# Kernel tuning notes

Hardware: AMD Instinct MI355X
Metric: run time of the kernel (lower is better)

Reference implementation:

```python
import jax, jax.numpy as jnp
import numpy as np

N, E, F_IN, HID, H, G = 50000, 800000, 128, 128, 4, 64
D = HID // H  # per-head dim = 32


def setup_inputs() -> dict:
    key = jax.random.key(0)
    ks = jax.random.split(key, 24)
    s = 0.05
    x = jax.random.normal(ks[0], (N, F_IN), dtype=jnp.float32)
    edge_index = jax.random.randint(ks[1], (2, E), 0, N, dtype=jnp.int64)
    batch = jnp.sort(jax.random.randint(ks[2], (N,), 0, G, dtype=jnp.int64))
    p = {}
    # layer 1: in F_IN -> H*D, layer 2: in HID -> H*D; each conv has q,k,v,skip linears (bias=True)
    names = ['Wq1', 'Wk1', 'Wv1', 'Ws1', 'Wq2', 'Wk2', 'Wv2', 'Ws2']
    dims = [(F_IN, HID)] * 4 + [(HID, HID)] * 4
    for i, (nm, dm) in enumerate(zip(names, dims)):
        p[nm] = jax.random.normal(ks[3 + 2 * i], dm, dtype=jnp.float32) * s
        p['b' + nm[1:]] = jax.random.normal(ks[4 + 2 * i], (dm[1],), dtype=jnp.float32) * s
    p['Wfc'] = jax.random.normal(ks[20], (HID, 1), dtype=jnp.float32) * s
    p['bfc'] = jax.random.normal(ks[21], (1,), dtype=jnp.float32) * s
    return {'x': x, 'edge_index': edge_index, 'batch': batch, **p}


def transformer_conv(x, edge_index, Wq, bq, Wk, bk, Wv, bv, Ws, bs):
    src, dst = edge_index[0], edge_index[1]  # messages flow src -> dst
    q = (x @ Wq + bq).reshape(-1, H, D)[dst]          # [E,H,D]
    k = (x @ Wk + bk).reshape(-1, H, D)[src]          # [E,H,D]
    v = (x @ Wv + bv).reshape(-1, H, D)[src]          # [E,H,D]
    logits = jnp.einsum('ehd,ehd->eh', q, k) / jnp.sqrt(jnp.float32(D))  # [E,H]
    m = jax.ops.segment_max(logits, dst, num_segments=N)                 # [N,H]
    e = jnp.exp(logits - m[dst])
    s = jax.ops.segment_sum(e, dst, num_segments=N)                      # [N,H]
    alpha = e / s[dst]
    agg = jax.ops.segment_sum(alpha[..., None] * v, dst, num_segments=N)  # [N,H,D]
    return agg.reshape(-1, HID) + (x @ Ws + bs)


def reference(x, edge_index, batch, Wq1, bq1, Wk1, bk1, Wv1, bv1, Ws1, bs1,
              Wq2, bq2, Wk2, bk2, Wv2, bv2, Ws2, bs2, Wfc, bfc):
    h = jax.nn.relu(transformer_conv(x, edge_index, Wq1, bq1, Wk1, bk1, Wv1, bv1, Ws1, bs1))
    h = jax.nn.relu(transformer_conv(h, edge_index, Wq2, bq2, Wk2, bk2, Wv2, bv2, Ws2, bs2))
    sums = jax.ops.segment_sum(h, batch, num_segments=G)                 # [G,HID]
    cnt = jax.ops.segment_sum(jnp.ones((h.shape[0],), h.dtype), batch, num_segments=G)
    pooled = sums / jnp.maximum(cnt, 1.0)[:, None]
    return (pooled @ Wfc + bfc).squeeze(-1)
```

## Files before the change

### kernel.cpp

```cpp
#include <hip/hip_runtime.h>
#include <hip/hip_bf16.h>
#include <math.h>

#define HID 128

typedef __attribute__((ext_vector_type(8))) short short8;
typedef __attribute__((ext_vector_type(4))) short short4v;
typedef __attribute__((ext_vector_type(4))) float f32x4;
typedef __attribute__((ext_vector_type(4))) int int4v;
typedef __attribute__((ext_vector_type(2))) unsigned int uint2v;
typedef __attribute__((ext_vector_type(4))) unsigned short ushort4v;
typedef __attribute__((ext_vector_type(2))) unsigned short ushort2v;
typedef __attribute__((ext_vector_type(2))) _Float16 half2v;

static inline size_t align256(size_t x){ return (x + 255) & ~(size_t)255; }

__device__ inline float bf2f(unsigned short h) {
  union { unsigned u; float f; } uf; uf.u = ((unsigned)h) << 16; return uf.f;
}
__device__ inline unsigned short f2bf(float f) {
  union { float f; unsigned u; } uf; uf.f = f;
  unsigned r = uf.u + 0x7fff + ((uf.u >> 16) & 1);
  return (unsigned short)(r >> 16);
}
__device__ inline unsigned short f2h(float f) {
  union { _Float16 h; unsigned short u; } c; c.h = (_Float16)f; return c.u;
}
__device__ inline half2v b2h2(unsigned u) {
  union { unsigned u; half2v h; } c; c.u = u; return c.h;
}

__device__ inline float dpp_rsum16(float x) {
  int v;
  v = __builtin_amdgcn_update_dpp(0, __float_as_int(x), 0xB1, 0xF, 0xF, true);
  x += __int_as_float(v);
  v = __builtin_amdgcn_update_dpp(0, __float_as_int(x), 0x4E, 0xF, 0xF, true);
  x += __int_as_float(v);
  v = __builtin_amdgcn_update_dpp(0, __float_as_int(x), 0x124, 0xF, 0xF, true);
  x += __int_as_float(v);
  v = __builtin_amdgcn_update_dpp(0, __float_as_int(x), 0x128, 0xF, 0xF, true);
  x += __int_as_float(v);
  return x;
}

__global__ __launch_bounds__(512) void k_prep(
    const float* W0, const float* W1, const float* W2, const float* W3,
    const float* W4, const float* W5, const float* W6, const float* W7,
    const float* b0, const float* b1, const float* b2, const float* b3,
    const float* b4, const float* b5, const float* b6, const float* b7,
    unsigned short* Wcat, float* Bcat,
    const int* __restrict__ edst, int* __restrict__ deg, int* __restrict__ rank, int e)
{
  __shared__ float tl[32][33];
  int t = threadIdx.x;
  if (blockIdx.x >= 128) {
    for (int i = (blockIdx.x - 128) * 512 + t; i < e; i += 512 * 512)
      rank[i] = atomicAdd(&deg[edst[i]], 1);
    return;
  }
  const float* Ws[8] = {W0, W1, W2, W3, W4, W5, W6, W7};
  const float* bs[8] = {b0, b1, b2, b3, b4, b5, b6, b7};
  int m = blockIdx.x >> 4, tile = blockIdx.x & 15;
  int tr = (tile >> 2) * 32, tc = (tile & 3) * 32;
  int tx = t & 31, ty = t >> 5;
  const float* Wm = Ws[m];
  #pragma unroll
  for (int r = 0; r < 32; r += 16) tl[ty + r][tx] = Wm[(tr + ty + r) * 128 + tc + tx];
  __syncthreads();
  #pragma unroll
  for (int r = 0; r < 32; r += 16)
    Wcat[m * 16384 + (tc + ty + r) * 128 + tr + tx] = f2bf(tl[tx][ty + r]);
  if (tile == 0 && t < 128) Bcat[m * 128 + t] = bs[m][t];
}

__global__ void k_scan_a(const int* __restrict__ deg, int* __restrict__ rowptr,
                         int* __restrict__ bsum, int n) {
  __shared__ int tmp[512];
  int t = threadIdx.x, i = blockIdx.x * 512 + t;
  int v = (i < n) ? deg[i] : 0;
  tmp[t] = v;
  __syncthreads();
  for (int off = 1; off < 512; off <<= 1) {
    int u = (t >= off) ? tmp[t - off] : 0;
    __syncthreads();
    tmp[t] += u;
    __syncthreads();
  }
  if (i < n) rowptr[i] = tmp[t] - v;
  if (t == 511) bsum[blockIdx.x] = tmp[t];
}

__global__ void k_scan_c(int* __restrict__ rowptr, const int* __restrict__ bsum,
                         int n, int e, int nb) {
  __shared__ int sred[8];
  __shared__ int base_sh;
  int t = threadIdx.x;
  int v = (t < nb && t < (int)blockIdx.x) ? bsum[t] : 0;
  #pragma unroll
  for (int off = 32; off >= 1; off >>= 1) v += __shfl_xor(v, off);
  if ((t & 63) == 0) sred[t >> 6] = v;
  __syncthreads();
  if (t == 0) {
    int b = 0;
    #pragma unroll
    for (int j = 0; j < 8; ++j) b += sred[j];
    base_sh = b;
  }
  __syncthreads();
  int i = blockIdx.x * 512 + t;
  if (i < n) rowptr[i] += base_sh;
  if (i == 0) rowptr[n] = e;
}

__global__ __launch_bounds__(256) void k_scatter(
    const int* __restrict__ esrc, const int* __restrict__ edst,
    const int* __restrict__ rowptr, const int* __restrict__ rank,
    int* __restrict__ csrc, int e)
{
  for (int i = blockIdx.x * 256 + threadIdx.x; i < e; i += gridDim.x * 256)
    csrc[rowptr[edst[i]] + rank[i]] = esrc[i] << 9;
}

template<int ABF16>
__global__ __launch_bounds__(256, 3) void k_qkvs(
    const void* __restrict__ Ain, const unsigned short* __restrict__ Wl,
    const float* __restrict__ Bl, unsigned short* __restrict__ Qb,
    unsigned short* __restrict__ KVb, unsigned short* __restrict__ Sb, int n)
{
  __shared__ unsigned short sA[64 * 128];
  __shared__ unsigned short sW[128 * 128];
  const int tid = threadIdx.x;
  const int rb = blockIdx.x * 64;
  const float QSC = 0.25503487f;

  if (ABF16) {
    const unsigned short* A = (const unsigned short*)Ain;
    #pragma unroll
    for (int it = 0; it < 4; ++it) {
      int q = tid + it * 256;
      int row = q >> 4, ch = q & 15;
      int gr = rb + row;
      short8 h = {0,0,0,0,0,0,0,0};
      if (gr < n) h = *reinterpret_cast<const short8*>(A + (size_t)gr * HID + ch * 8);
      *reinterpret_cast<short8*>(&sA[row * 128 + ((ch ^ (row & 7)) << 3)]) = h;
    }
  } else {
    const float* A = (const float*)Ain;
    #pragma unroll
    for (int it = 0; it < 8; ++it) {
      int q = tid + it * 256;
      int row = q >> 5, c4 = (q & 31) * 4;
      int gr = rb + row;
      f32x4 a = {0.f, 0.f, 0.f, 0.f};
      if (gr < n) a = *reinterpret_cast<const f32x4*>(A + (size_t)gr * HID + c4);
      short4v h;
      h.x = (short)f2bf(a.x); h.y = (short)f2bf(a.y);
      h.z = (short)f2bf(a.z); h.w = (short)f2bf(a.w);
      int eloff = row * 128 + (((c4 >> 3) ^ (row & 7)) << 3) + (c4 & 7);
      *reinterpret_cast<short4v*>(&sA[eloff]) = h;
    }
  }

  const int lane = tid & 63;
  const int wv = tid >> 6;

  auto stageW = [&](int y) {
    const unsigned short* Wy = Wl + (size_t)y * 16384;
    #pragma unroll
    for (int it = 0; it < 8; ++it) {
      int q = tid + it * 256;
      int c = q >> 4, ch = q & 15;
      short8 w = *reinterpret_cast<const short8*>(Wy + c * 128 + ch * 8);
      *reinterpret_cast<short8*>(&sW[c * 128 + ((ch ^ (c & 7)) << 3)]) = w;
    }
  };

  stageW(0);
  __syncthreads();

  short8 af[4];
  #pragma unroll
  for (int ks = 0; ks < 4; ++ks) {
    int ch = ks * 4 + (lane >> 4);
    int row = wv * 16 + (lane & 15);
    af[ks] = *reinterpret_cast<const short8*>(&sA[row * 128 + ((ch ^ (row & 7)) << 3)]);
  }

  f32x4 acc[8];
  auto compute = [&]() {
    #pragma unroll
    for (int mf = 0; mf < 8; ++mf) acc[mf] = (f32x4){0.f, 0.f, 0.f, 0.f};
    #pragma unroll
    for (int ks = 0; ks < 4; ++ks) {
      int ch = ks * 4 + (lane >> 4);
      short8 wf[8];
      #pragma unroll
      for (int mf = 0; mf < 8; ++mf) {
        int wc = mf * 16 + (lane & 15);
        wf[mf] = *reinterpret_cast<const short8*>(&sW[wc * 128 + ((ch ^ (wc & 7)) << 3)]);
      }
      #pragma unroll
      for (int mf = 0; mf < 8; ++mf)
        acc[mf] = __builtin_amdgcn_mfma_f32_16x16x32_bf16(wf[mf], af[ks], acc[mf], 0, 0, 0);
    }
  };

  const int gr = rb + wv * 16 + (lane & 15);
  const int cbase = (lane >> 4) << 2;

  compute();
  if (gr < n) {
    #pragma unroll
    for (int mf = 0; mf < 8; ++mf) {
      int c0 = mf * 16 + cbase;
      f32x4 b = *reinterpret_cast<const f32x4*>(Bl + 0 * 128 + c0);
      f32x4 v = acc[mf];
      ushort4v h;
      h.x = f2h((v.x + b.x) * QSC); h.y = f2h((v.y + b.y) * QSC);
      h.z = f2h((v.z + b.z) * QSC); h.w = f2h((v.w + b.w) * QSC);
      *reinterpret_cast<ushort4v*>(Qb + (size_t)gr * HID + c0) = h;
    }
  }

  __syncthreads();
  stageW(3);
  __syncthreads();
  compute();
  if (gr < n) {
    #pragma unroll
    for (int mf = 0; mf < 8; ++mf) {
      int c0 = mf * 16 + cbase;
      f32x4 b = *reinterpret_cast<const f32x4*>(Bl + 3 * 128 + c0);
      f32x4 v = acc[mf];
      ushort4v h;
      h.x = f2h(v.x + b.x); h.y = f2h(v.y + b.y);
      h.z = f2h(v.z + b.z); h.w = f2h(v.w + b.w);
      *reinterpret_cast<ushort4v*>(Sb + (size_t)gr * HID + c0) = h;
    }
  }

  __syncthreads();
  stageW(1);
  __syncthreads();
  compute();
  f32x4 kacc[8];
  #pragma unroll
  for (int mf = 0; mf < 8; ++mf) kacc[mf] = acc[mf];

  __syncthreads();
  stageW(2);
  __syncthreads();
  compute();
  if (gr < n) {
    #pragma unroll
    for (int mf = 0; mf < 8; ++mf) {
      int c0 = mf * 16 + cbase;
      f32x4 bk = *reinterpret_cast<const f32x4*>(Bl + 1 * 128 + c0);
      f32x4 bv = *reinterpret_cast<const f32x4*>(Bl + 2 * 128 + c0);
      f32x4 kv = kacc[mf], vv = acc[mf];
      short8 h;
      h[0] = (short)f2h(kv.x + bk.x); h[1] = (short)f2h(kv.y + bk.y);
      h[2] = (short)f2h(vv.x + bv.x); h[3] = (short)f2h(vv.y + bv.y);
      h[4] = (short)f2h(kv.z + bk.z); h[5] = (short)f2h(kv.w + bk.w);
      h[6] = (short)f2h(vv.z + bv.z); h[7] = (short)f2h(vv.w + bv.w);
      *reinterpret_cast<short8*>(KVb + (size_t)gr * 256 + 2 * c0) = h;
    }
  }
}

__global__ __launch_bounds__(256, 8) void k_attn2(
    const unsigned short* __restrict__ Qb, const unsigned short* __restrict__ KVb,
    const unsigned short* __restrict__ Sb, const int* __restrict__ rowptr,
    const int* __restrict__ csrc, unsigned short* __restrict__ Hout, int n)
{
  int wid = blockIdx.x * 4 + (threadIdx.x >> 6);
  if (wid >= n) return;
  int lane = threadIdx.x & 63;
  half2v qh = b2h2(*reinterpret_cast<const unsigned*>(Qb + (size_t)wid * HID + 2 * lane));
  int e0 = rowptr[wid], deg = rowptr[wid + 1] - e0;
  const int* cp = csrc + e0;
  const char* kvb = (const char*)KVb + lane * 8;
  float m = -INFINITY, s = 0.f, a0 = 0.f, a1 = 0.f;

  auto LDo = [&](int off) -> uint2v {
    return *reinterpret_cast<const uint2v*>(kvb + (unsigned)off);
  };
  auto proc1 = [&](uint2v kv) {
    float lg = dpp_rsum16(__builtin_amdgcn_fdot2(qh, b2h2(kv.x), 0.f, false));
    if (!__all(lg <= m + 11.5f)) {
      float nm = fmaxf(m, lg);
      float cc = __builtin_amdgcn_exp2f(m - nm);
      s *= cc; a0 *= cc; a1 *= cc; m = nm;
    }
    float p = __builtin_amdgcn_exp2f(lg - m);
    half2v vh = b2h2(kv.y);
    s += p;
    a0 = fmaf(p, (float)vh.x, a0);
    a1 = fmaf(p, (float)vh.y, a1);
  };
  auto proc4 = [&](uint2v e0v, uint2v e1v, uint2v e2v, uint2v e3v) {
    float l0 = dpp_rsum16(__builtin_amdgcn_fdot2(qh, b2h2(e0v.x), 0.f, false));
    float l1 = dpp_rsum16(__builtin_amdgcn_fdot2(qh, b2h2(e1v.x), 0.f, false));
    float l2 = dpp_rsum16(__builtin_amdgcn_fdot2(qh, b2h2(e2v.x), 0.f, false));
    float l3 = dpp_rsum16(__builtin_amdgcn_fdot2(qh, b2h2(e3v.x), 0.f, false));
    float qm = fmaxf(fmaxf(l0, l1), fmaxf(l2, l3));
    if (!__all(qm <= m + 11.5f)) {
      float nm = fmaxf(m, qm);
      float cc = __builtin_amdgcn_exp2f(m - nm);
      s *= cc; a0 *= cc; a1 *= cc; m = nm;
    }
    float p0 = __builtin_amdgcn_exp2f(l0 - m);
    float p1 = __builtin_amdgcn_exp2f(l1 - m);
    float p2 = __builtin_amdgcn_exp2f(l2 - m);
    float p3 = __builtin_amdgcn_exp2f(l3 - m);
    s += (p0 + p1) + (p2 + p3);
    half2v v0 = b2h2(e0v.y), v1 = b2h2(e1v.y), v2 = b2h2(e2v.y), v3 = b2h2(e3v.y);
    a0 = fmaf(p3, (float)v3.x, fmaf(p2, (float)v2.x, fmaf(p1, (float)v1.x, fmaf(p0, (float)v0.x, a0))));
    a1 = fmaf(p3, (float)v3.y, fmaf(p2, (float)v2.y, fmaf(p1, (float)v1.y, fmaf(p0, (float)v0.y, a1))));
  };

  int nq = deg >> 2, r = deg & 3;
  if (nq) {
    int4v o; __builtin_memcpy(&o, cp, 16);
    uint2v b0 = LDo(o.x), b1 = LDo(o.y), b2 = LDo(o.z), b3 = LDo(o.w);
    for (int q = 1; q < nq; ++q) {
      int4v no; __builtin_memcpy(&no, cp + 4 * q, 16);
      uint2v n0 = LDo(no.x), n1 = LDo(no.y), n2 = LDo(no.z), n3 = LDo(no.w);
      proc4(b0, b1, b2, b3);
      b0 = n0; b1 = n1; b2 = n2; b3 = n3;
    }
    proc4(b0, b1, b2, b3);
  }
  int tb = nq * 4;
  for (int i = 0; i < r; ++i) proc1(LDo(cp[tb + i]));

  float inv = (s > 0.f) ? 1.f / s : 0.f;
  half2v sh = b2h2(*reinterpret_cast<const unsigned*>(Sb + (size_t)wid * HID + 2 * lane));
  ushort2v h;
  h.x = f2bf(fmaxf(fmaf(a0, inv, (float)sh.x), 0.f));
  h.y = f2bf(fmaxf(fmaf(a1, inv, (float)sh.y), 0.f));
  *reinterpret_cast<ushort2v*>(Hout + (size_t)wid * HID + 2 * lane) = h;
}

__global__ __launch_bounds__(256) void k_poolfc(
    const unsigned short* __restrict__ H, const int* __restrict__ batch,
    const float* __restrict__ Wfc, const float* __restrict__ bfc,
    float* __restrict__ out, int n)
{
  int g = blockIdx.x;
  int lo = 0, hi = n;
  while (lo < hi) { int mid = (lo + hi) >> 1; if (batch[mid] < g) lo = mid + 1; else hi = mid; }
  int start = lo;
  hi = n;
  while (lo < hi) { int mid = (lo + hi) >> 1; if (batch[mid] < g + 1) lo = mid + 1; else hi = mid; }
  int end = lo;

  int t = threadIdx.x;
  int col = t & 127, rr = t >> 7;
  float a0 = 0.f, a1 = 0.f, a2 = 0.f, a3 = 0.f;
  int i = start + rr;
  for (; i + 6 < end; i += 8) {
    a0 += bf2f(H[(size_t)i * HID + col]);
    a1 += bf2f(H[(size_t)(i + 2) * HID + col]);
    a2 += bf2f(H[(size_t)(i + 4) * HID + col]);
    a3 += bf2f(H[(size_t)(i + 6) * HID + col]);
  }
  for (; i < end; i += 2) a0 += bf2f(H[(size_t)i * HID + col]);
  float v = ((a0 + a1) + (a2 + a3)) * Wfc[col];

  __shared__ float red[4];
  #pragma unroll
  for (int off = 32; off >= 1; off >>= 1) v += __shfl_xor(v, off);
  if ((t & 63) == 0) red[t >> 6] = v;
  __syncthreads();
  if (t == 0) {
    float tot = (red[0] + red[1]) + (red[2] + red[3]);
    float cnt = (float)(end - start);
    out[g] = tot / fmaxf(cnt, 1.f) + bfc[0];
  }
}

extern "C" void kernel_launch(void* const* d_in, const int* in_sizes, int n_in,
                              void* d_out, int out_size, void* d_ws, size_t ws_size,
                              hipStream_t stream)
{
  const float* x   = (const float*)d_in[0];
  const int*   ei  = (const int*)d_in[1];
  const int*   bat = (const int*)d_in[2];
  const float *Wq1 = (const float*)d_in[3],  *bq1 = (const float*)d_in[4];
  const float *Wk1 = (const float*)d_in[5],  *bk1 = (const float*)d_in[6];
  const float *Wv1 = (const float*)d_in[7],  *bv1 = (const float*)d_in[8];
  const float *Ws1 = (const float*)d_in[9],  *bs1 = (const float*)d_in[10];
  const float *Wq2 = (const float*)d_in[11], *bq2 = (const float*)d_in[12];
  const float *Wk2 = (const float*)d_in[13], *bk2 = (const float*)d_in[14];
  const float *Wv2 = (const float*)d_in[15], *bv2 = (const float*)d_in[16];
  const float *Ws2 = (const float*)d_in[17], *bs2 = (const float*)d_in[18];
  const float *Wfc = (const float*)d_in[19], *bfc = (const float*)d_in[20];
  float* out = (float*)d_out;

  const int N = in_sizes[0] / HID;
  const int E = in_sizes[1] / 2;
  const int G = 64;

  char* p = (char*)d_ws;
  auto alloc = [&](size_t bytes) -> char* { char* r = p; p += align256(bytes); return r; };
  unsigned short* Qb  = (unsigned short*)alloc((size_t)N * HID * 2);
  unsigned short* KVb = (unsigned short*)alloc((size_t)N * 256 * 2);
  unsigned short* Sb  = (unsigned short*)alloc((size_t)N * HID * 2);
  unsigned short* Hb  = (unsigned short*)alloc((size_t)N * HID * 2);
  unsigned short* H2b = (unsigned short*)alloc((size_t)N * HID * 2);
  unsigned short* Wcat = (unsigned short*)alloc((size_t)8 * 128 * 128 * 2);
  float* Bcat = (float*)alloc((size_t)8 * 128 * 4);
  int* rowptr = (int*)alloc((size_t)(N + 1) * sizeof(int));
  int* deg    = (int*)alloc((size_t)N * sizeof(int));
  int* rank   = (int*)alloc((size_t)E * sizeof(int));
  int* bsum   = (int*)alloc(4096);
  int* csrc   = (int*)alloc((size_t)E * sizeof(int));

  const int* esrc = ei;
  const int* edst = ei + E;

  hipMemsetAsync(deg, 0, (size_t)N * sizeof(int), stream);

  k_prep<<<640, 512, 0, stream>>>(
      Wq1, Wk1, Wv1, Ws1, Wq2, Wk2, Wv2, Ws2,
      bq1, bk1, bv1, bs1, bq2, bk2, bv2, bs2,
      Wcat, Bcat, edst, deg, rank, E);

  int SB = (N + 511) / 512;
  k_scan_a<<<SB, 512, 0, stream>>>(deg, rowptr, bsum, N);
  k_scan_c<<<SB, 512, 0, stream>>>(rowptr, bsum, N, E, SB);
  k_scatter<<<512, 256, 0, stream>>>(esrc, edst, rowptr, rank, csrc, E);

  int QB = (N + 63) / 64;
  k_qkvs<0><<<QB, 256, 0, stream>>>(x, Wcat, Bcat, Qb, KVb, Sb, N);
  k_attn2<<<(N + 3) / 4, 256, 0, stream>>>(Qb, KVb, Sb, rowptr, csrc, Hb, N);
  k_qkvs<1><<<QB, 256, 0, stream>>>(Hb, Wcat + 4 * 16384, Bcat + 512, Qb, KVb, Sb, N);
  k_attn2<<<(N + 3) / 4, 256, 0, stream>>>(Qb, KVb, Sb, rowptr, csrc, H2b, N);
  k_poolfc<<<G, 256, 0, stream>>>(H2b, bat, Wfc, bfc, out, N);
}
```

Measured before the change: 365.9 us.

## Split attention wave into two half-waves processing alternate edges with wider loads

The per-node attention kernel now gives each 32-lane half of a wavefront every other incoming edge. Each lane loads 16 bytes of interleaved K/V (4 channels) instead of 8, and the per-head dot-product reduction is shortened to 8 lanes. The two halves keep independent online-softmax states and merge them with cross-half shuffles at the end. The KV producer's layout is reordered to match, and the occupancy hint drops from 8 to 6 blocks to allow more registers. This is meant to halve per-edge instruction overhead and double bytes per gather. The cost is extra merge work and idle lanes on odd degrees.

New measurement: 364.7 us. No clear change (-0.3%).

```diff
diff --git a/kernel.cpp b/kernel.cpp
--- a/kernel.cpp
+++ b/kernel.cpp
@@ -8,7 +8,7 @@
 typedef __attribute__((ext_vector_type(4))) short short4v;
 typedef __attribute__((ext_vector_type(4))) float f32x4;
 typedef __attribute__((ext_vector_type(4))) int int4v;
-typedef __attribute__((ext_vector_type(2))) unsigned int uint2v;
+typedef __attribute__((ext_vector_type(4))) unsigned int uint4v;
 typedef __attribute__((ext_vector_type(4))) unsigned short ushort4v;
 typedef __attribute__((ext_vector_type(2))) unsigned short ushort2v;
 typedef __attribute__((ext_vector_type(2))) _Float16 half2v;
@@ -30,15 +30,13 @@
   union { unsigned u; half2v h; } c; c.u = u; return c.h;
 }
 
-__device__ inline float dpp_rsum16(float x) {
+__device__ inline float dpp_rsum8(float x) {
   int v;
   v = __builtin_amdgcn_update_dpp(0, __float_as_int(x), 0xB1, 0xF, 0xF, true);
   x += __int_as_float(v);
   v = __builtin_amdgcn_update_dpp(0, __float_as_int(x), 0x4E, 0xF, 0xF, true);
   x += __int_as_float(v);
-  v = __builtin_amdgcn_update_dpp(0, __float_as_int(x), 0x124, 0xF, 0xF, true);
-  x += __int_as_float(v);
-  v = __builtin_amdgcn_update_dpp(0, __float_as_int(x), 0x128, 0xF, 0xF, true);
+  v = __builtin_amdgcn_update_dpp(0, __float_as_int(x), 0x141, 0xF, 0xF, true);
   x += __int_as_float(v);
   return x;
 }
@@ -260,86 +258,128 @@
       f32x4 kv = kacc[mf], vv = acc[mf];
       short8 h;
       h[0] = (short)f2h(kv.x + bk.x); h[1] = (short)f2h(kv.y + bk.y);
-      h[2] = (short)f2h(vv.x + bv.x); h[3] = (short)f2h(vv.y + bv.y);
-      h[4] = (short)f2h(kv.z + bk.z); h[5] = (short)f2h(kv.w + bk.w);
+      h[2] = (short)f2h(kv.z + bk.z); h[3] = (short)f2h(kv.w + bk.w);
+      h[4] = (short)f2h(vv.x + bv.x); h[5] = (short)f2h(vv.y + bv.y);
       h[6] = (short)f2h(vv.z + bv.z); h[7] = (short)f2h(vv.w + bv.w);
       *reinterpret_cast<short8*>(KVb + (size_t)gr * 256 + 2 * c0) = h;
     }
   }
 }
 
-__global__ __launch_bounds__(256, 8) void k_attn2(
+__global__ __launch_bounds__(256, 6) void k_attn2(
     const unsigned short* __restrict__ Qb, const unsigned short* __restrict__ KVb,
     const unsigned short* __restrict__ Sb, const int* __restrict__ rowptr,
     const int* __restrict__ csrc, unsigned short* __restrict__ Hout, int n)
 {
   int wid = blockIdx.x * 4 + (threadIdx.x >> 6);
   if (wid >= n) return;
-  int lane = threadIdx.x & 63;
-  half2v qh = b2h2(*reinterpret_cast<const unsigned*>(Qb + (size_t)wid * HID + 2 * lane));
+  const int lane = threadIdx.x & 63;
+  const int l32 = lane & 31;
+  const int half = lane >> 5;
+
+  uint2 qu = *reinterpret_cast<const uint2*>(Qb + (size_t)wid * HID + 4 * l32);
+  half2v qh0 = b2h2(qu.x), qh1 = b2h2(qu.y);
+
   int e0 = rowptr[wid], deg = rowptr[wid + 1] - e0;
   const int* cp = csrc + e0;
-  const char* kvb = (const char*)KVb + lane * 8;
-  float m = -INFINITY, s = 0.f, a0 = 0.f, a1 = 0.f;
-
-  auto LDo = [&](int off) -> uint2v {
-    return *reinterpret_cast<const uint2v*>(kvb + (unsigned)off);
-  };
-  auto proc1 = [&](uint2v kv) {
-    float lg = dpp_rsum16(__builtin_amdgcn_fdot2(qh, b2h2(kv.x), 0.f, false));
+  const char* kvb = (const char*)KVb + l32 * 16;
+
+  float m = -INFINITY, s = 0.f;
+  float a0 = 0.f, a1 = 0.f, a2 = 0.f, a3 = 0.f;
+
+  auto LDo = [&](int off) -> uint4v {
+    return *reinterpret_cast<const uint4v*>(kvb + (unsigned)off);
+  };
+  auto logit = [&](uint4v kv) -> float {
+    float d = __builtin_amdgcn_fdot2(qh1, b2h2(kv.y),
+              __builtin_amdgcn_fdot2(qh0, b2h2(kv.x), 0.f, false), false);
+    return dpp_rsum8(d);
+  };
+  auto accum = [&](float p, uint4v kv) {
+    half2v v0 = b2h2(kv.z), v1 = b2h2(kv.w);
+    a0 = fmaf(p, (float)v0.x, a0);
+    a1 = fmaf(p, (float)v0.y, a1);
+    a2 = fmaf(p, (float)v1.x, a2);
+    a3 = fmaf(p, (float)v1.y, a3);
+  };
+  auto procB = [&](uint4v kvA, uint4v kvB) {
+    float lA = logit(kvA), lB = logit(kvB);
+    float qm = fmaxf(lA, lB);
+    if (!__all(qm <= m + 11.5f)) {
+      float nm = fmaxf(m, qm);
+      float cc = __builtin_amdgcn_exp2f(m - nm);
+      s *= cc; a0 *= cc; a1 *= cc; a2 *= cc; a3 *= cc; m = nm;
+    }
+    float pA = __builtin_amdgcn_exp2f(lA - m);
+    float pB = __builtin_amdgcn_exp2f(lB - m);
+    s += pA + pB;
+    accum(pA, kvA);
+    accum(pB, kvB);
+  };
+  auto proc1 = [&](int idx0) {
+    int idx = idx0 + half;
+    bool valid = idx < deg;
+    uint4v kv = LDo(valid ? cp[idx] : 0);
+    float lg = logit(kv);
+    lg = valid ? lg : -INFINITY;
     if (!__all(lg <= m + 11.5f)) {
       float nm = fmaxf(m, lg);
       float cc = __builtin_amdgcn_exp2f(m - nm);
-      s *= cc; a0 *= cc; a1 *= cc; m = nm;
-    }
-    float p = __builtin_amdgcn_exp2f(lg - m);
-    half2v vh = b2h2(kv.y);
+      s *= cc; a0 *= cc; a1 *= cc; a2 *= cc; a3 *= cc; m = nm;
+    }
+    float p = valid ? __builtin_amdgcn_exp2f(lg - m) : 0.f;
     s += p;
-    a0 = fmaf(p, (float)vh.x, a0);
-    a1 = fmaf(p, (float)vh.y, a1);
-  };
-  auto proc4 = [&](uint2v e0v, uint2v e1v, uint2v e2v, uint2v e3v) {
-    float l0 = dpp_rsum16(__builtin_amdgcn_fdot2(qh, b2h2(e0v.x), 0.f, false));
-    float l1 = dpp_rsum16(__builtin_amdgcn_fdot2(qh, b2h2(e1v.x), 0.f, false));
-    float l2 = dpp_rsum16(__builtin_amdgcn_fdot2(qh, b2h2(e2v.x), 0.f, false));
-    float l3 = dpp_rsum16(__builtin_amdgcn_fdot2(qh, b2h2(e3v.x), 0.f, false));
-    float qm = fmaxf(fmaxf(l0, l1), fmaxf(l2, l3));
-    if (!__all(qm <= m + 11.5f)) {
-      float nm = fmaxf(m, qm);
-      float cc = __builtin_amdgcn_exp2f(m - nm);
-      s *= cc; a0 *= cc; a1 *= cc; m = nm;
-    }
-    float p0 = __builtin_amdgcn_exp2f(l0 - m);
-    float p1 = __builtin_amdgcn_exp2f(l1 - m);
-    float p2 = __builtin_amdgcn_exp2f(l2 - m);
-    float p3 = __builtin_amdgcn_exp2f(l3 - m);
-    s += (p0 + p1) + (p2 + p3);
-    half2v v0 = b2h2(e0v.y), v1 = b2h2(e1v.y), v2 = b2h2(e2v.y), v3 = b2h2(e3v.y);
-    a0 = fmaf(p3, (float)v3.x, fmaf(p2, (float)v2.x, fmaf(p1, (float)v1.x, fmaf(p0, (float)v0.x, a0))));
-    a1 = fmaf(p3, (float)v3.y, fmaf(p2, (float)v2.y, fmaf(p1, (float)v1.y, fmaf(p0, (float)v0.y, a1))));
-  };
-
-  int nq = deg >> 2, r = deg & 3;
-  if (nq) {
-    int4v o; __builtin_memcpy(&o, cp, 16);
-    uint2v b0 = LDo(o.x), b1 = LDo(o.y), b2 = LDo(o.z), b3 = LDo(o.w);
-    for (int q = 1; q < nq; ++q) {
-      int4v no; __builtin_memcpy(&no, cp + 4 * q, 16);
-      uint2v n0 = LDo(no.x), n1 = LDo(no.y), n2 = LDo(no.z), n3 = LDo(no.w);
-      proc4(b0, b1, b2, b3);
-      b0 = n0; b1 = n1; b2 = n2; b3 = n3;
-    }
-    proc4(b0, b1, b2, b3);
-  }
-  int tb = nq * 4;
-  for (int i = 0; i < r; ++i) proc1(LDo(cp[tb + i]));
-
-  float inv = (s > 0.f) ? 1.f / s : 0.f;
-  half2v sh = b2h2(*reinterpret_cast<const unsigned*>(Sb + (size_t)wid * HID + 2 * lane));
-  ushort2v h;
-  h.x = f2bf(fmaxf(fmaf(a0, inv, (float)sh.x), 0.f));
-  h.y = f2bf(fmaxf(fmaf(a1, inv, (float)sh.y), 0.f));
-  *reinterpret_cast<ushort2v*>(Hout + (size_t)wid * HID + 2 * lane) = h;
+    accum(p, kv);
+  };
+
+  int nb = deg >> 2;
+  if (nb >= 2) {
+    int oA0 = cp[0 + half], oA1 = cp[2 + half];
+    int oB0 = cp[4 + half], oB1 = cp[6 + half];
+    uint4v A0 = LDo(oA0), A1 = LDo(oA1);
+    uint4v B0 = LDo(oB0), B1 = LDo(oB1);
+    for (int b = 2; b < nb; ++b) {
+      int base = 4 * b;
+      int n0 = cp[base + half], n1 = cp[base + 2 + half];
+      uint4v N0 = LDo(n0), N1 = LDo(n1);
+      procB(A0, A1);
+      A0 = B0; A1 = B1;
+      B0 = N0; B1 = N1;
+    }
+    procB(A0, A1);
+    procB(B0, B1);
+  } else if (nb == 1) {
+    procB(LDo(cp[half]), LDo(cp[2 + half]));
+  }
+  int tb = nb * 4, rem = deg - tb;
+  if (rem > 0) proc1(tb);
+  if (rem > 2) proc1(tb + 2);
+
+  float mo = __shfl_xor(m, 32);
+  float so = __shfl_xor(s, 32);
+  float b0 = __shfl_xor(a0, 32), b1 = __shfl_xor(a1, 32);
+  float b2 = __shfl_xor(a2, 32), b3 = __shfl_xor(a3, 32);
+  float M = fmaxf(m, mo);
+  float c0 = (m  > -INFINITY) ? __builtin_amdgcn_exp2f(m  - M) : 0.f;
+  float c1 = (mo > -INFINITY) ? __builtin_amdgcn_exp2f(mo - M) : 0.f;
+  float st = s * c0 + so * c1;
+  float inv = (st > 0.f) ? 1.f / st : 0.f;
+  float r0 = (a0 * c0 + b0 * c1) * inv;
+  float r1 = (a1 * c0 + b1 * c1) * inv;
+  float r2 = (a2 * c0 + b2 * c1) * inv;
+  float r3 = (a3 * c0 + b3 * c1) * inv;
+
+  if (half == 0) {
+    ushort4v sh = *reinterpret_cast<const ushort4v*>(Sb + (size_t)wid * HID + 4 * l32);
+    half2v s0 = b2h2((unsigned)sh.x | ((unsigned)sh.y << 16));
+    half2v s1 = b2h2((unsigned)sh.z | ((unsigned)sh.w << 16));
+    ushort4v h;
+    h.x = f2bf(fmaxf(r0 + (float)s0.x, 0.f));
+    h.y = f2bf(fmaxf(r1 + (float)s0.y, 0.f));
+    h.z = f2bf(fmaxf(r2 + (float)s1.x, 0.f));
+    h.w = f2bf(fmaxf(r3 + (float)s1.y, 0.f));
+    *reinterpret_cast<ushort4v*>(Hout + (size_t)wid * HID + 4 * l32) = h;
+  }
 }
 
 __global__ __launch_bounds__(256) void k_poolfc(
```
